# Optimization experiments

Measured on AMD Instinct MI355X. Metric: run time of the kernel, lower is better.

The kernel has to match this reference:

```python
import jax, jax.numpy as jnp
import numpy as np

D_MODEL = 1024
D_STATE = 16
D_CONV = 4
EXPAND = 2
D_INNER = EXPAND * D_MODEL          # 2048
DT_RANK = D_MODEL // 16             # 64 ('auto' in mamba_ssm)
B_SZ = 2
SEQ = 1024


def setup_inputs() -> dict:
    key = jax.random.key(0)
    ks = jax.random.split(key, 8)
    g = lambda k, shape, scale: (jax.random.normal(k, shape, dtype=jnp.float32) * scale)
    x = jax.random.normal(ks[0], (B_SZ, SEQ, D_MODEL), dtype=jnp.float32)
    in_proj_w = g(ks[1], (2 * D_INNER, D_MODEL), D_MODEL ** -0.5)
    conv_w = g(ks[2], (D_INNER, 1, D_CONV), D_CONV ** -0.5)
    conv_b = jnp.zeros((D_INNER,), jnp.float32)
    x_proj_w = g(ks[3], (DT_RANK + 2 * D_STATE, D_INNER), D_INNER ** -0.5)
    dt_proj_w = g(ks[4], (D_INNER, DT_RANK), DT_RANK ** -0.5)
    # dt bias initialized so softplus(bias) ~ [1e-3, 0.1] like mamba_ssm
    dt_proj_b = jax.random.uniform(ks[5], (D_INNER,), jnp.float32, -6.0, -2.0)
    # S4D-real init: A = -(1..d_state) per channel
    A_log = jnp.log(jnp.tile(jnp.arange(1, D_STATE + 1, dtype=jnp.float32), (D_INNER, 1)))
    D = jnp.ones((D_INNER,), jnp.float32)
    out_proj_w = g(ks[6], (D_MODEL, D_INNER), D_INNER ** -0.5)
    return dict(x=x, in_proj_w=in_proj_w, conv_w=conv_w, conv_b=conv_b,
                x_proj_w=x_proj_w, dt_proj_w=dt_proj_w, dt_proj_b=dt_proj_b,
                A_log=A_log, D=D, out_proj_w=out_proj_w)


def _mamba(x, in_proj_w, conv_w, conv_b, x_proj_w, dt_proj_w, dt_proj_b, A_log, D, out_proj_w):
    Bt, L, _ = x.shape
    # input projection -> [B, L, 2*d_inner], split into conv branch u and gate z
    xz = jnp.einsum('bld,ed->ble', x, in_proj_w)
    u, z = jnp.split(xz, 2, axis=-1)
    # causal depthwise conv1d over time
    uc = jnp.transpose(u, (0, 2, 1))  # [B, d_inner, L]
    uc = jax.lax.conv_general_dilated(
        uc, conv_w, window_strides=(1,), padding=[(D_CONV - 1, 0)],
        feature_group_count=D_INNER, dimension_numbers=('NCH', 'OIH', 'NCH'))
    u = jax.nn.silu(jnp.transpose(uc, (0, 2, 1)) + conv_b)  # [B, L, d_inner]
    # data-dependent SSM parameters
    x_dbl = jnp.einsum('bld,ed->ble', u, x_proj_w)  # [B, L, dt_rank + 2*d_state]
    dt, Bmat, Cmat = jnp.split(x_dbl, [DT_RANK, DT_RANK + D_STATE], axis=-1)
    delta = jax.nn.softplus(jnp.einsum('blr,dr->bld', dt, dt_proj_w) + dt_proj_b)
    A = -jnp.exp(A_log)  # [d_inner, d_state], strictly negative

    def step(h, inp):
        d_t, B_t, C_t, u_t = inp  # [B,d_inner],[B,d_state],[B,d_state],[B,d_inner]
        dA = jnp.exp(d_t[:, :, None] * A)                       # [B, d_inner, d_state]
        h = dA * h + (d_t * u_t)[:, :, None] * B_t[:, None, :]  # discretized update
        y = jnp.einsum('bdn,bn->bd', h, C_t)
        return h, y

    h0 = jnp.zeros((Bt, D_INNER, D_STATE), x.dtype)
    xs = (jnp.swapaxes(delta, 0, 1), jnp.swapaxes(Bmat, 0, 1),
          jnp.swapaxes(Cmat, 0, 1), jnp.swapaxes(u, 0, 1))
    _, ys = jax.lax.scan(step, h0, xs)
    y = jnp.swapaxes(ys, 0, 1) + u * D   # skip connection D*u
    y = y * jax.nn.silu(z)               # gated output
    return jnp.einsum('bld,ed->ble', y, out_proj_w)


def reference(x, in_proj_w, conv_w, conv_b, x_proj_w, dt_proj_w, dt_proj_b, A_log, D, out_proj_w):
    # ResidualMamba: x + Mamba(x)
    return x + _mamba(x, in_proj_w, conv_w, conv_b, x_proj_w, dt_proj_w, dt_proj_b, A_log, D, out_proj_w)
```

## Files before the change

kernel.cpp:

```cpp
#include <hip/hip_runtime.h>
#include <hip/hip_bf16.h>
#include <math.h>

#define D_MODEL 1024
#define D_STATE 16
#define D_CONV  4
#define D_INNER 2048
#define DT_RANK 64
#define B_SZ    2
#define SEQ     1024
#define ML      (B_SZ * SEQ)

typedef unsigned short ushort_t;
typedef __attribute__((ext_vector_type(8))) short s8v;
typedef __attribute__((ext_vector_type(4))) float f4v;

__device__ __forceinline__ float softplus_f(float v) {
    return (v > 20.f) ? v : log1pf(__expf(v));
}

__global__ __launch_bounds__(256) void split_bf16_tiled(
    const float* __restrict__ A, ushort_t* __restrict__ H, ushort_t* __restrict__ L,
    int Kd, int ktlog, int total)
{
    int t = blockIdx.x * 256 + threadIdx.x;
    if (t >= total) return;
    int kslot = t & 3;
    int r  = (t >> 2) & 127;
    int tl = t >> 9;
    int kt = tl & ((1 << ktlog) - 1);
    int rt = tl >> ktlog;
    int row = rt * 128 + r;
    int col = (kt << 5) + kslot * 8;

    const float* src = &A[(size_t)row * Kd + col];
    float4 v0 = *reinterpret_cast<const float4*>(src);
    float4 v1 = *reinterpret_cast<const float4*>(src + 4);
    float f[8] = {v0.x, v0.y, v0.z, v0.w, v1.x, v1.y, v1.z, v1.w};
    s8v hv, lv;
#pragma unroll
    for (int j = 0; j < 8; ++j) {
        unsigned int ub = __float_as_uint(f[j]);
        unsigned int hb = (ub + 0x7fffu + ((ub >> 16) & 1u)) >> 16;
        float hf = __uint_as_float(hb << 16);
        float g  = f[j] - hf;
        unsigned int ug = __float_as_uint(g);
        unsigned int lb = (ug + 0x7fffu + ((ug >> 16) & 1u)) >> 16;
        hv[j] = (short)hb;
        lv[j] = (short)lb;
    }
    *reinterpret_cast<s8v*>(&H[(size_t)t * 8]) = hv;
    *reinterpret_cast<s8v*>(&L[(size_t)t * 8]) = lv;
}

template <int WTM, bool RES>
__global__ __launch_bounds__(256) void gemm_mfma_split(
    const ushort_t* __restrict__ Ah, const ushort_t* __restrict__ Al,
    const ushort_t* __restrict__ Bh, const ushort_t* __restrict__ Bl,
    const float* __restrict__ Rres,
    float* __restrict__ C, int ldc, int K)
{
    constexpr int BM  = WTM * 32;
    constexpr int CPW = BM / 64;
    __shared__ short AhL[BM * 32], AlL[BM * 32];
    __shared__ short BhL[128 * 32], BlL[128 * 32];

    const int tid = threadIdx.x;
    const int l = tid & 63;
    const int w = tid >> 6;
    const int m0 = blockIdx.y * BM;
    const int n0 = blockIdx.x * 128;
    const int wm = (w >> 1) * (WTM * 16);
    const int wn = (w & 1) * 64;

    const int ktiles = K >> 5;
    size_t abase = (size_t)(m0 >> 7) * ktiles * 4096 + (size_t)(m0 & 127) * 32;
    size_t bbase = (size_t)(n0 >> 7) * ktiles * 4096;

    f4v acc[WTM][4] = {};

    for (int kt = 0; kt < ktiles; ++kt) {
#pragma unroll
        for (int i = 0; i < CPW; ++i) {
            int ci = w * CPW + i;
            __builtin_amdgcn_global_load_lds(
                (const __attribute__((address_space(1))) unsigned int*)(Ah + abase + ci * 512 + l * 8),
                (__attribute__((address_space(3))) unsigned int*)&AhL[ci * 512], 16, 0, 0);
            __builtin_amdgcn_global_load_lds(
                (const __attribute__((address_space(1))) unsigned int*)(Al + abase + ci * 512 + l * 8),
                (__attribute__((address_space(3))) unsigned int*)&AlL[ci * 512], 16, 0, 0);
        }
#pragma unroll
        for (int i = 0; i < 2; ++i) {
            int ci = w * 2 + i;
            __builtin_amdgcn_global_load_lds(
                (const __attribute__((address_space(1))) unsigned int*)(Bh + bbase + ci * 512 + l * 8),
                (__attribute__((address_space(3))) unsigned int*)&BhL[ci * 512], 16, 0, 0);
            __builtin_amdgcn_global_load_lds(
                (const __attribute__((address_space(1))) unsigned int*)(Bl + bbase + ci * 512 + l * 8),
                (__attribute__((address_space(3))) unsigned int*)&BlL[ci * 512], 16, 0, 0);
        }
        asm volatile("s_waitcnt vmcnt(0)" ::: "memory");
        __syncthreads();

        s8v fah[WTM], fal[WTM], fbh[4], fbl[4];
        const int fo = (l & 15) * 32 + (l >> 4) * 8;
#pragma unroll
        for (int tr = 0; tr < WTM; ++tr) {
            fah[tr] = *reinterpret_cast<const s8v*>(&AhL[(wm + tr * 16) * 32 + fo]);
            fal[tr] = *reinterpret_cast<const s8v*>(&AlL[(wm + tr * 16) * 32 + fo]);
        }
#pragma unroll
        for (int tc = 0; tc < 4; ++tc) {
            fbh[tc] = *reinterpret_cast<const s8v*>(&BhL[(wn + tc * 16) * 32 + fo]);
            fbl[tc] = *reinterpret_cast<const s8v*>(&BlL[(wn + tc * 16) * 32 + fo]);
        }

#pragma unroll
        for (int tr = 0; tr < WTM; ++tr)
#pragma unroll
            for (int tc = 0; tc < 4; ++tc) {
                f4v c = acc[tr][tc];
                c = __builtin_amdgcn_mfma_f32_16x16x32_bf16(fah[tr], fbh[tc], c, 0, 0, 0);
                c = __builtin_amdgcn_mfma_f32_16x16x32_bf16(fah[tr], fbl[tc], c, 0, 0, 0);
                c = __builtin_amdgcn_mfma_f32_16x16x32_bf16(fal[tr], fbh[tc], c, 0, 0, 0);
                acc[tr][tc] = c;
            }
        __syncthreads();
        abase += 4096;
        bbase += 4096;
    }

    const int mb = m0 + wm + ((l >> 4) << 2);
    const int nb = n0 + wn + (l & 15);
#pragma unroll
    for (int tr = 0; tr < WTM; ++tr)
#pragma unroll
        for (int tc = 0; tc < 4; ++tc)
#pragma unroll
            for (int r = 0; r < 4; ++r) {
                int m = mb + tr * 16 + r;
                int n = nb + tc * 16;
                float v = acc[tr][tc][r];
                if (RES) v += Rres[(size_t)m * ldc + n];
                C[(size_t)m * ldc + n] = v;
            }
}

template <int BM, int BN, int TM, int TN, int ACT, bool BIAS>
__global__ __launch_bounds__(256) void gemm_tn(
    const float* __restrict__ A, int lda,
    const float* __restrict__ W, int ldw,
    const float* __restrict__ bias,
    float* __restrict__ C, int ldc,
    int K)
{
    constexpr int BK = 16;
    constexpr int LDA_S = BM + 4;
    constexpr int LDB_S = BN + 4;
    constexpr int RSUB = TM / 4;
    constexpr int CSUB = TN / 4;
    constexpr int NTX = BN / TN;
    constexpr int AF4 = BM * 4 / 256;
    constexpr int BF4 = BN * 4 / 256;
    static_assert((BM / TM) * (BN / TN) == 256, "256 threads");

    __shared__ float As[BK][LDA_S];
    __shared__ float Bs[BK][LDB_S];

    const int tid = threadIdx.x;
    const int tx = tid % NTX;
    const int ty = tid / NTX;
    const int m0 = blockIdx.y * BM;
    const int n0 = blockIdx.x * BN;

    float acc[TM][TN] = {};
    float4 pa[AF4], pb[BF4];

#pragma unroll
    for (int i = 0; i < AF4; ++i) {
        int f = tid + i * 256, row = f >> 2, kq = f & 3;
        pa[i] = *reinterpret_cast<const float4*>(&A[(size_t)(m0 + row) * lda + kq * 4]);
    }
#pragma unroll
    for (int i = 0; i < BF4; ++i) {
        int f = tid + i * 256, row = f >> 2, kq = f & 3;
        pb[i] = *reinterpret_cast<const float4*>(&W[(size_t)(n0 + row) * ldw + kq * 4]);
    }

    for (int k0 = 0; k0 < K; k0 += BK) {
#pragma unroll
        for (int i = 0; i < AF4; ++i) {
            int f = tid + i * 256, row = f >> 2, kq = f & 3;
            As[kq * 4 + 0][row] = pa[i].x; As[kq * 4 + 1][row] = pa[i].y;
            As[kq * 4 + 2][row] = pa[i].z; As[kq * 4 + 3][row] = pa[i].w;
        }
#pragma unroll
        for (int i = 0; i < BF4; ++i) {
            int f = tid + i * 256, row = f >> 2, kq = f & 3;
            Bs[kq * 4 + 0][row] = pb[i].x; Bs[kq * 4 + 1][row] = pb[i].y;
            Bs[kq * 4 + 2][row] = pb[i].z; Bs[kq * 4 + 3][row] = pb[i].w;
        }
        __syncthreads();

        if (k0 + BK < K) {
#pragma unroll
            for (int i = 0; i < AF4; ++i) {
                int f = tid + i * 256, row = f >> 2, kq = f & 3;
                pa[i] = *reinterpret_cast<const float4*>(&A[(size_t)(m0 + row) * lda + k0 + BK + kq * 4]);
            }
#pragma unroll
            for (int i = 0; i < BF4; ++i) {
                int f = tid + i * 256, row = f >> 2, kq = f & 3;
                pb[i] = *reinterpret_cast<const float4*>(&W[(size_t)(n0 + row) * ldw + k0 + BK + kq * 4]);
            }
        }

#pragma unroll
        for (int kk = 0; kk < BK; ++kk) {
            float a[TM], b[TN];
#pragma unroll
            for (int r = 0; r < RSUB; ++r) {
                float4 av = *reinterpret_cast<const float4*>(&As[kk][r * (BM / RSUB) + ty * 4]);
                a[r * 4 + 0] = av.x; a[r * 4 + 1] = av.y; a[r * 4 + 2] = av.z; a[r * 4 + 3] = av.w;
            }
#pragma unroll
            for (int c = 0; c < CSUB; ++c) {
                float4 bv = *reinterpret_cast<const float4*>(&Bs[kk][c * (BN / CSUB) + tx * 4]);
                b[c * 4 + 0] = bv.x; b[c * 4 + 1] = bv.y; b[c * 4 + 2] = bv.z; b[c * 4 + 3] = bv.w;
            }
#pragma unroll
            for (int i = 0; i < TM; ++i)
#pragma unroll
                for (int j = 0; j < TN; ++j)
                    acc[i][j] = fmaf(a[i], b[j], acc[i][j]);
        }
        __syncthreads();
    }

#pragma unroll
    for (int i = 0; i < TM; ++i) {
        int r = i >> 2, ii = i & 3;
        int m = m0 + r * (BM / RSUB) + ty * 4 + ii;
#pragma unroll
        for (int c = 0; c < CSUB; ++c) {
            int n = n0 + c * (BN / CSUB) + tx * 4;
            float v0 = acc[i][c * 4 + 0], v1 = acc[i][c * 4 + 1];
            float v2 = acc[i][c * 4 + 2], v3 = acc[i][c * 4 + 3];
            if (BIAS) {
                float4 b4 = *reinterpret_cast<const float4*>(&bias[n]);
                v0 += b4.x; v1 += b4.y; v2 += b4.z; v3 += b4.w;
            }
            if (ACT == 1) {
                v0 = softplus_f(v0); v1 = softplus_f(v1);
                v2 = softplus_f(v2); v3 = softplus_f(v3);
            }
            *reinterpret_cast<float4*>(&C[(size_t)m * ldc + n]) = make_float4(v0, v1, v2, v3);
        }
    }
}

__global__ __launch_bounds__(256) void conv_silu(
    const float* __restrict__ xz,
    const float* __restrict__ cw,
    const float* __restrict__ cb,
    float* __restrict__ u)
{
    int idx = blockIdx.x * 256 + threadIdx.x;
    if (idx >= ML * (D_INNER / 4)) return;
    int d4  = idx & (D_INNER / 4 - 1);
    int row = idx >> 9;
    int l   = row & (SEQ - 1);

    const float* base = xz + (size_t)row * 4096 + d4 * 4;
    float xr[4][4];
    {
        float4 v = *reinterpret_cast<const float4*>(base);
        xr[0][0] = v.x; xr[0][1] = v.y; xr[0][2] = v.z; xr[0][3] = v.w;
    }
#pragma unroll
    for (int t = 1; t < 4; ++t) {
        float4 v = make_float4(0.f, 0.f, 0.f, 0.f);
        if (l >= t) v = *reinterpret_cast<const float4*>(base - (size_t)t * 4096);
        xr[t][0] = v.x; xr[t][1] = v.y; xr[t][2] = v.z; xr[t][3] = v.w;
    }
    float4 b4 = *reinterpret_cast<const float4*>(&cb[d4 * 4]);
    float bb[4] = {b4.x, b4.y, b4.z, b4.w};
    float out[4];
#pragma unroll
    for (int c = 0; c < 4; ++c) {
        float4 w = *reinterpret_cast<const float4*>(&cw[(d4 * 4 + c) * 4]);
        float s = bb[c];
        s = fmaf(w.w, xr[0][c], s);
        s = fmaf(w.z, xr[1][c], s);
        s = fmaf(w.y, xr[2][c], s);
        s = fmaf(w.x, xr[3][c], s);
        out[c] = s / (1.f + __expf(-s));
    }
    *reinterpret_cast<float4*>(&u[(size_t)row * 2048 + d4 * 4]) =
        make_float4(out[0], out[1], out[2], out[3]);
}

__global__ __launch_bounds__(256) void xproj_partial(
    const float* __restrict__ u,
    const float* __restrict__ W,
    float* __restrict__ part)
{
    __shared__ float Us[64][36];
    __shared__ float Ws[96][36];
    const int tid = threadIdx.x;
    const int tx = tid & 31;
    const int ty = tid >> 5;
    const int r0 = blockIdx.x * 64;
    const int kbase = blockIdx.y * 256;

    float acc[8][3] = {};

    for (int kc = kbase; kc < kbase + 256; kc += 32) {
#pragma unroll
        for (int i = 0; i < 2; ++i) {
            int f = tid + i * 256, row = f >> 3, kq = f & 7;
            *reinterpret_cast<float4*>(&Us[row][kq * 4]) =
                *reinterpret_cast<const float4*>(&u[(size_t)(r0 + row) * 2048 + kc + kq * 4]);
        }
#pragma unroll
        for (int i = 0; i < 3; ++i) {
            int f = tid + i * 256, row = f >> 3, kq = f & 7;
            *reinterpret_cast<float4*>(&Ws[row][kq * 4]) =
                *reinterpret_cast<const float4*>(&W[(size_t)row * 2048 + kc + kq * 4]);
        }
        __syncthreads();
#pragma unroll
        for (int k4 = 0; k4 < 32; k4 += 4) {
            float4 wv[3];
#pragma unroll
            for (int j = 0; j < 3; ++j)
                wv[j] = *reinterpret_cast<const float4*>(&Ws[tx + 32 * j][k4]);
#pragma unroll
            for (int i = 0; i < 8; ++i) {
                float4 uv = *reinterpret_cast<const float4*>(&Us[ty * 8 + i][k4]);
#pragma unroll
                for (int j = 0; j < 3; ++j) {
                    acc[i][j] = fmaf(uv.x, wv[j].x, acc[i][j]);
                    acc[i][j] = fmaf(uv.y, wv[j].y, acc[i][j]);
                    acc[i][j] = fmaf(uv.z, wv[j].z, acc[i][j]);
                    acc[i][j] = fmaf(uv.w, wv[j].w, acc[i][j]);
                }
            }
        }
        __syncthreads();
    }
#pragma unroll
    for (int i = 0; i < 8; ++i)
#pragma unroll
        for (int j = 0; j < 3; ++j)
            part[((size_t)blockIdx.y * ML + r0 + ty * 8 + i) * 96 + tx + 32 * j] = acc[i][j];
}

__global__ __launch_bounds__(256) void xproj_reduce(
    const float* __restrict__ part,
    float* __restrict__ xdbl)
{
    int i = blockIdx.x * 256 + threadIdx.x;
    if (i >= ML * 96 / 4) return;
    const float4* p4 = reinterpret_cast<const float4*>(part);
    float4 s = p4[i];
#pragma unroll
    for (int sgl = 1; sgl < 8; ++sgl) {
        float4 v = p4[(size_t)sgl * (ML * 96 / 4) + i];
        s.x += v.x; s.y += v.y; s.z += v.z; s.w += v.w;
    }
    reinterpret_cast<float4*>(xdbl)[i] = s;
}

#define CH 64

__device__ __forceinline__ float dpp_add(float x, const int ctrl_unused) { return x; }

__global__ __launch_bounds__(256) void scan_kernel(
    const float* __restrict__ delta,
    const float* __restrict__ u,
    const float* __restrict__ xdbl,
    const float* __restrict__ xz,
    const float* __restrict__ A_log,
    const float* __restrict__ Dvec,
    float* __restrict__ yg)
{
    __shared__ __align__(16) float sd[16][CH + 4], su[16][CH + 4],
                                   sB[16][CH + 4], sC[16][CH + 4];
    __shared__ __align__(16) float sy[CH][20];

    const int tid = threadIdx.x;
    const int b   = blockIdx.x >> 7;
    const int d0  = (blockIdx.x & 127) * 16;
    const int dch = tid >> 4;
    const int n   = tid & 15;

    const int sc4 = (tid & 3) * 4;
    const int slr = tid >> 2;

    const float Aval = -expf(A_log[(d0 + dch) * 16 + n]);
    const float Dsel = (n == 15) ? Dvec[d0 + dch] : 0.f;
    float h = 0.f;

    for (int l0 = 0; l0 < SEQ; l0 += CH) {
        {
            int row = b * SEQ + l0 + slr;
            float4 dv = *reinterpret_cast<const float4*>(&delta[(size_t)row * 2048 + d0 + sc4]);
            float4 uv = *reinterpret_cast<const float4*>(&u[(size_t)row * 2048 + d0 + sc4]);
            float4 Bv = *reinterpret_cast<const float4*>(&xdbl[(size_t)row * 96 + 64 + sc4]);
            float4 Cv = *reinterpret_cast<const float4*>(&xdbl[(size_t)row * 96 + 80 + sc4]);
            sd[sc4 + 0][slr] = dv.x; sd[sc4 + 1][slr] = dv.y; sd[sc4 + 2][slr] = dv.z; sd[sc4 + 3][slr] = dv.w;
            su[sc4 + 0][slr] = uv.x; su[sc4 + 1][slr] = uv.y; su[sc4 + 2][slr] = uv.z; su[sc4 + 3][slr] = uv.w;
            sB[sc4 + 0][slr] = Bv.x; sB[sc4 + 1][slr] = Bv.y; sB[sc4 + 2][slr] = Bv.z; sB[sc4 + 3][slr] = Bv.w;
            sC[sc4 + 0][slr] = Cv.x; sC[sc4 + 1][slr] = Cv.y; sC[sc4 + 2][slr] = Cv.z; sC[sc4 + 3][slr] = Cv.w;
        }
        __syncthreads();

        float pbuf[8];
#pragma unroll 2
        for (int l8 = 0; l8 < CH; l8 += 8) {
#pragma unroll
            for (int g = 0; g < 2; ++g) {
                const int l4 = l8 + g * 4;
                float4 d4 = *reinterpret_cast<const float4*>(&sd[dch][l4]);
                float4 u4 = *reinterpret_cast<const float4*>(&su[dch][l4]);
                float4 B4 = *reinterpret_cast<const float4*>(&sB[n][l4]);
                float4 C4 = *reinterpret_cast<const float4*>(&sC[n][l4]);
                float dts[4] = {d4.x, d4.y, d4.z, d4.w};
                float uus[4] = {u4.x, u4.y, u4.z, u4.w};
                float Bs4[4] = {B4.x, B4.y, B4.z, B4.w};
                float Cs4[4] = {C4.x, C4.y, C4.z, C4.w};
#pragma unroll
                for (int j = 0; j < 4; ++j) {
                    float dt = dts[j];
                    float dA = __expf(dt * Aval);
                    h = fmaf(dA, h, dt * uus[j] * Bs4[j]);
                    pbuf[g * 4 + j] = fmaf(uus[j], Dsel, h * Cs4[j]);
                }
            }
#pragma unroll
            for (int j = 0; j < 8; ++j) {
                float p = pbuf[j];
                p += __int_as_float(__builtin_amdgcn_update_dpp(0, __float_as_int(p), 0x111, 0xf, 0xf, true));
                p += __int_as_float(__builtin_amdgcn_update_dpp(0, __float_as_int(p), 0x112, 0xf, 0xf, true));
                p += __int_as_float(__builtin_amdgcn_update_dpp(0, __float_as_int(p), 0x114, 0xf, 0xf, true));
                p += __int_as_float(__builtin_amdgcn_update_dpp(0, __float_as_int(p), 0x118, 0xf, 0xf, true));
                pbuf[j] = p;
            }
            if (n == 15) {
#pragma unroll
                for (int j = 0; j < 8; ++j) sy[l8 + j][dch] = pbuf[j];
            }
        }
        __syncthreads();

        {
            int row = b * SEQ + l0 + slr;
            float4 ps = *reinterpret_cast<const float4*>(&sy[slr][sc4]);
            float4 zv = *reinterpret_cast<const float4*>(&xz[(size_t)row * 4096 + 2048 + d0 + sc4]);
            float o[4];
            float pp[4] = {ps.x, ps.y, ps.z, ps.w};
            float zzv[4] = {zv.x, zv.y, zv.z, zv.w};
#pragma unroll
            for (int q = 0; q < 4; ++q) {
                float zz = zzv[q];
                o[q] = pp[q] * (zz / (1.f + __expf(-zz)));
            }
            *reinterpret_cast<float4*>(&yg[(size_t)row * 2048 + d0 + sc4]) =
                make_float4(o[0], o[1], o[2], o[3]);
        }
        __syncthreads();
    }
}

extern "C" void kernel_launch(void* const* d_in, const int* in_sizes, int n_in,
                              void* d_out, int out_size, void* d_ws, size_t ws_size,
                              hipStream_t stream)
{
    const float* x         = (const float*)d_in[0];
    const float* in_proj_w = (const float*)d_in[1];
    const float* conv_w    = (const float*)d_in[2];
    const float* conv_b    = (const float*)d_in[3];
    const float* x_proj_w  = (const float*)d_in[4];
    const float* dt_proj_w = (const float*)d_in[5];
    const float* dt_proj_b = (const float*)d_in[6];
    const float* A_log     = (const float*)d_in[7];
    const float* Dvec      = (const float*)d_in[8];
    const float* out_proj_w= (const float*)d_in[9];
    float* out = (float*)d_out;

    float* ws    = (float*)d_ws;
    float* xz    = ws;
    float* u     = ws + 8388608;
    float* xdbl  = ws + 12582912;
    float* delta = ws + 12779520;
    float* part  = delta;
    float* yg    = ws + 16973824;

    ushort_t* bfb = (ushort_t*)(ws + 21168128);
    ushort_t* Xh  = bfb;
    ushort_t* Xl  = bfb + 2097152;
    ushort_t* Wih = bfb + 4194304;
    ushort_t* Wil = bfb + 8388608;
    ushort_t* Ygh = bfb;
    ushort_t* Ygl = bfb + 4194304;
    ushort_t* Woh = bfb + 8388608;
    ushort_t* Wol = bfb + 10485760;

    split_bf16_tiled<<<dim3(1024), 256, 0, stream>>>(x, Xh, Xl, 1024, 5, ML * 1024 / 8);
    split_bf16_tiled<<<dim3(2048), 256, 0, stream>>>(in_proj_w, Wih, Wil, 1024, 5, 4096 * 1024 / 8);

    gemm_mfma_split<4, false><<<dim3(32, 16), 256, 0, stream>>>(
        Xh, Xl, Wih, Wil, nullptr, xz, 4096, 1024);

    conv_silu<<<dim3(ML * (D_INNER / 4) / 256), 256, 0, stream>>>(xz, conv_w, conv_b, u);

    xproj_partial<<<dim3(32, 8), 256, 0, stream>>>(u, x_proj_w, part);
    xproj_reduce<<<dim3((ML * 96 / 4 + 255) / 256), 256, 0, stream>>>(part, xdbl);

    gemm_tn<128, 128, 8, 8, 1, true><<<dim3(16, 16), 256, 0, stream>>>(
        xdbl, 96, dt_proj_w, 64, dt_proj_b, delta, 2048, 64);

    scan_kernel<<<dim3(256), 256, 0, stream>>>(delta, u, xdbl, xz, A_log, Dvec, yg);

    split_bf16_tiled<<<dim3(2048), 256, 0, stream>>>(yg, Ygh, Ygl, 2048, 6, ML * 2048 / 8);
    split_bf16_tiled<<<dim3(1024), 256, 0, stream>>>(out_proj_w, Woh, Wol, 2048, 6, 1024 * 2048 / 8);

    gemm_mfma_split<2, true><<<dim3(8, 32), 256, 0, stream>>>(
        Ygh, Ygl, Woh, Wol, x, out, 1024, 2048);
}
```

Baseline: 385.2 us.

## Fuse dt_proj GEMM and softplus into the selective scan kernel

Drops the separate dt_proj GEMM and its 16 MB delta buffer. Each scan block now loads its 16 rows of dt_proj_w plus bias into shared memory, and for every 64-step chunk computes delta = softplus(dt·W + b) from the dt slice of xdbl. This removes a kernel launch and a full write and read of delta through global memory. The cost is extra FMA work and an extra barrier per chunk inside the latency-bound scan, which runs only 256 blocks.

```diff
diff --git a/kernel.cpp b/kernel.cpp
--- a/kernel.cpp
+++ b/kernel.cpp
@@ -147,119 +147,6 @@
             }
 }
 
-template <int BM, int BN, int TM, int TN, int ACT, bool BIAS>
-__global__ __launch_bounds__(256) void gemm_tn(
-    const float* __restrict__ A, int lda,
-    const float* __restrict__ W, int ldw,
-    const float* __restrict__ bias,
-    float* __restrict__ C, int ldc,
-    int K)
-{
-    constexpr int BK = 16;
-    constexpr int LDA_S = BM + 4;
-    constexpr int LDB_S = BN + 4;
-    constexpr int RSUB = TM / 4;
-    constexpr int CSUB = TN / 4;
-    constexpr int NTX = BN / TN;
-    constexpr int AF4 = BM * 4 / 256;
-    constexpr int BF4 = BN * 4 / 256;
-    static_assert((BM / TM) * (BN / TN) == 256, "256 threads");
-
-    __shared__ float As[BK][LDA_S];
-    __shared__ float Bs[BK][LDB_S];
-
-    const int tid = threadIdx.x;
-    const int tx = tid % NTX;
-    const int ty = tid / NTX;
-    const int m0 = blockIdx.y * BM;
-    const int n0 = blockIdx.x * BN;
-
-    float acc[TM][TN] = {};
-    float4 pa[AF4], pb[BF4];
-
-#pragma unroll
-    for (int i = 0; i < AF4; ++i) {
-        int f = tid + i * 256, row = f >> 2, kq = f & 3;
-        pa[i] = *reinterpret_cast<const float4*>(&A[(size_t)(m0 + row) * lda + kq * 4]);
-    }
-#pragma unroll
-    for (int i = 0; i < BF4; ++i) {
-        int f = tid + i * 256, row = f >> 2, kq = f & 3;
-        pb[i] = *reinterpret_cast<const float4*>(&W[(size_t)(n0 + row) * ldw + kq * 4]);
-    }
-
-    for (int k0 = 0; k0 < K; k0 += BK) {
-#pragma unroll
-        for (int i = 0; i < AF4; ++i) {
-            int f = tid + i * 256, row = f >> 2, kq = f & 3;
-            As[kq * 4 + 0][row] = pa[i].x; As[kq * 4 + 1][row] = pa[i].y;
-            As[kq * 4 + 2][row] = pa[i].z; As[kq * 4 + 3][row] = pa[i].w;
-        }
-#pragma unroll
-        for (int i = 0; i < BF4; ++i) {
-            int f = tid + i * 256, row = f >> 2, kq = f & 3;
-            Bs[kq * 4 + 0][row] = pb[i].x; Bs[kq * 4 + 1][row] = pb[i].y;
-            Bs[kq * 4 + 2][row] = pb[i].z; Bs[kq * 4 + 3][row] = pb[i].w;
-        }
-        __syncthreads();
-
-        if (k0 + BK < K) {
-#pragma unroll
-            for (int i = 0; i < AF4; ++i) {
-                int f = tid + i * 256, row = f >> 2, kq = f & 3;
-                pa[i] = *reinterpret_cast<const float4*>(&A[(size_t)(m0 + row) * lda + k0 + BK + kq * 4]);
-            }
-#pragma unroll
-            for (int i = 0; i < BF4; ++i) {
-                int f = tid + i * 256, row = f >> 2, kq = f & 3;
-                pb[i] = *reinterpret_cast<const float4*>(&W[(size_t)(n0 + row) * ldw + k0 + BK + kq * 4]);
-            }
-        }
-
-#pragma unroll
-        for (int kk = 0; kk < BK; ++kk) {
-            float a[TM], b[TN];
-#pragma unroll
-            for (int r = 0; r < RSUB; ++r) {
-                float4 av = *reinterpret_cast<const float4*>(&As[kk][r * (BM / RSUB) + ty * 4]);
-                a[r * 4 + 0] = av.x; a[r * 4 + 1] = av.y; a[r * 4 + 2] = av.z; a[r * 4 + 3] = av.w;
-            }
-#pragma unroll
-            for (int c = 0; c < CSUB; ++c) {
-                float4 bv = *reinterpret_cast<const float4*>(&Bs[kk][c * (BN / CSUB) + tx * 4]);
-                b[c * 4 + 0] = bv.x; b[c * 4 + 1] = bv.y; b[c * 4 + 2] = bv.z; b[c * 4 + 3] = bv.w;
-            }
-#pragma unroll
-            for (int i = 0; i < TM; ++i)
-#pragma unroll
-                for (int j = 0; j < TN; ++j)
-                    acc[i][j] = fmaf(a[i], b[j], acc[i][j]);
-        }
-        __syncthreads();
-    }
-
-#pragma unroll
-    for (int i = 0; i < TM; ++i) {
-        int r = i >> 2, ii = i & 3;
-        int m = m0 + r * (BM / RSUB) + ty * 4 + ii;
-#pragma unroll
-        for (int c = 0; c < CSUB; ++c) {
-            int n = n0 + c * (BN / CSUB) + tx * 4;
-            float v0 = acc[i][c * 4 + 0], v1 = acc[i][c * 4 + 1];
-            float v2 = acc[i][c * 4 + 2], v3 = acc[i][c * 4 + 3];
-            if (BIAS) {
-                float4 b4 = *reinterpret_cast<const float4*>(&bias[n]);
-                v0 += b4.x; v1 += b4.y; v2 += b4.z; v3 += b4.w;
-            }
-            if (ACT == 1) {
-                v0 = softplus_f(v0); v1 = softplus_f(v1);
-                v2 = softplus_f(v2); v3 = softplus_f(v3);
-            }
-            *reinterpret_cast<float4*>(&C[(size_t)m * ldc + n]) = make_float4(v0, v1, v2, v3);
-        }
-    }
-}
-
 __global__ __launch_bounds__(256) void conv_silu(
     const float* __restrict__ xz,
     const float* __restrict__ cw,
@@ -375,19 +262,21 @@
 
 #define CH 64
 
-__device__ __forceinline__ float dpp_add(float x, const int ctrl_unused) { return x; }
-
 __global__ __launch_bounds__(256) void scan_kernel(
-    const float* __restrict__ delta,
     const float* __restrict__ u,
     const float* __restrict__ xdbl,
     const float* __restrict__ xz,
     const float* __restrict__ A_log,
     const float* __restrict__ Dvec,
+    const float* __restrict__ dtw,
+    const float* __restrict__ dtb,
     float* __restrict__ yg)
 {
-    __shared__ __align__(16) float sd[16][CH + 4], su[16][CH + 4],
+    __shared__ __align__(16) float sdt[CH][68];
+    __shared__ __align__(16) float sdel[16][CH + 4], su16[16][CH + 4],
                                    sB[16][CH + 4], sC[16][CH + 4];
+    __shared__ __align__(16) float dtw_s[16][68];
+    __shared__ float db_s[16];
     __shared__ __align__(16) float sy[CH][20];
 
     const int tid = threadIdx.x;
@@ -399,21 +288,61 @@
     const int sc4 = (tid & 3) * 4;
     const int slr = tid >> 2;
 
+    {
+        int r = tid >> 4, c4 = (tid & 15) * 4;
+        *reinterpret_cast<float4*>(&dtw_s[r][c4]) =
+            *reinterpret_cast<const float4*>(&dtw[(size_t)(d0 + r) * 64 + c4]);
+        if (tid < 16) db_s[tid] = dtb[d0 + tid];
+    }
     const float Aval = -expf(A_log[(d0 + dch) * 16 + n]);
     const float Dsel = (n == 15) ? Dvec[d0 + dch] : 0.f;
     float h = 0.f;
+    __syncthreads();
 
     for (int l0 = 0; l0 < SEQ; l0 += CH) {
         {
+#pragma unroll
+            for (int i = 0; i < 4; ++i) {
+                int idx = tid + i * 256;
+                int rr = idx >> 4, c4 = (idx & 15) * 4;
+                *reinterpret_cast<float4*>(&sdt[rr][c4]) =
+                    *reinterpret_cast<const float4*>(&xdbl[(size_t)(b * SEQ + l0 + rr) * 96 + c4]);
+            }
             int row = b * SEQ + l0 + slr;
-            float4 dv = *reinterpret_cast<const float4*>(&delta[(size_t)row * 2048 + d0 + sc4]);
             float4 uv = *reinterpret_cast<const float4*>(&u[(size_t)row * 2048 + d0 + sc4]);
             float4 Bv = *reinterpret_cast<const float4*>(&xdbl[(size_t)row * 96 + 64 + sc4]);
             float4 Cv = *reinterpret_cast<const float4*>(&xdbl[(size_t)row * 96 + 80 + sc4]);
-            sd[sc4 + 0][slr] = dv.x; sd[sc4 + 1][slr] = dv.y; sd[sc4 + 2][slr] = dv.z; sd[sc4 + 3][slr] = dv.w;
-            su[sc4 + 0][slr] = uv.x; su[sc4 + 1][slr] = uv.y; su[sc4 + 2][slr] = uv.z; su[sc4 + 3][slr] = uv.w;
-            sB[sc4 + 0][slr] = Bv.x; sB[sc4 + 1][slr] = Bv.y; sB[sc4 + 2][slr] = Bv.z; sB[sc4 + 3][slr] = Bv.w;
-            sC[sc4 + 0][slr] = Cv.x; sC[sc4 + 1][slr] = Cv.y; sC[sc4 + 2][slr] = Cv.z; sC[sc4 + 3][slr] = Cv.w;
+            su16[sc4 + 0][slr] = uv.x; su16[sc4 + 1][slr] = uv.y;
+            su16[sc4 + 2][slr] = uv.z; su16[sc4 + 3][slr] = uv.w;
+            sB[sc4 + 0][slr] = Bv.x; sB[sc4 + 1][slr] = Bv.y;
+            sB[sc4 + 2][slr] = Bv.z; sB[sc4 + 3][slr] = Bv.w;
+            sC[sc4 + 0][slr] = Cv.x; sC[sc4 + 1][slr] = Cv.y;
+            sC[sc4 + 2][slr] = Cv.z; sC[sc4 + 3][slr] = Cv.w;
+        }
+        __syncthreads();
+
+        {
+            float4 s0 = make_float4(0.f, 0.f, 0.f, 0.f), s1 = s0, s2 = s0, s3 = s0;
+#pragma unroll
+            for (int k4 = 0; k4 < 64; k4 += 4) {
+                float4 dv = *reinterpret_cast<const float4*>(&sdt[slr][k4]);
+                float4 w0 = *reinterpret_cast<const float4*>(&dtw_s[sc4 + 0][k4]);
+                float4 w1 = *reinterpret_cast<const float4*>(&dtw_s[sc4 + 1][k4]);
+                float4 w2 = *reinterpret_cast<const float4*>(&dtw_s[sc4 + 2][k4]);
+                float4 w3 = *reinterpret_cast<const float4*>(&dtw_s[sc4 + 3][k4]);
+                s0.x = fmaf(dv.x, w0.x, s0.x); s0.y = fmaf(dv.y, w0.y, s0.y);
+                s0.z = fmaf(dv.z, w0.z, s0.z); s0.w = fmaf(dv.w, w0.w, s0.w);
+                s1.x = fmaf(dv.x, w1.x, s1.x); s1.y = fmaf(dv.y, w1.y, s1.y);
+                s1.z = fmaf(dv.z, w1.z, s1.z); s1.w = fmaf(dv.w, w1.w, s1.w);
+                s2.x = fmaf(dv.x, w2.x, s2.x); s2.y = fmaf(dv.y, w2.y, s2.y);
+                s2.z = fmaf(dv.z, w2.z, s2.z); s2.w = fmaf(dv.w, w2.w, s2.w);
+                s3.x = fmaf(dv.x, w3.x, s3.x); s3.y = fmaf(dv.y, w3.y, s3.y);
+                s3.z = fmaf(dv.z, w3.z, s3.z); s3.w = fmaf(dv.w, w3.w, s3.w);
+            }
+            sdel[sc4 + 0][slr] = softplus_f((s0.x + s0.y) + (s0.z + s0.w) + db_s[sc4 + 0]);
+            sdel[sc4 + 1][slr] = softplus_f((s1.x + s1.y) + (s1.z + s1.w) + db_s[sc4 + 1]);
+            sdel[sc4 + 2][slr] = softplus_f((s2.x + s2.y) + (s2.z + s2.w) + db_s[sc4 + 2]);
+            sdel[sc4 + 3][slr] = softplus_f((s3.x + s3.y) + (s3.z + s3.w) + db_s[sc4 + 3]);
         }
         __syncthreads();
 
@@ -423,8 +352,8 @@
 #pragma unroll
             for (int g = 0; g < 2; ++g) {
                 const int l4 = l8 + g * 4;
-                float4 d4 = *reinterpret_cast<const float4*>(&sd[dch][l4]);
-                float4 u4 = *reinterpret_cast<const float4*>(&su[dch][l4]);
+                float4 d4 = *reinterpret_cast<const float4*>(&sdel[dch][l4]);
+                float4 u4 = *reinterpret_cast<const float4*>(&su16[dch][l4]);
                 float4 B4 = *reinterpret_cast<const float4*>(&sB[n][l4]);
                 float4 C4 = *reinterpret_cast<const float4*>(&sC[n][l4]);
                 float dts[4] = {d4.x, d4.y, d4.z, d4.w};
@@ -494,8 +423,7 @@
     float* xz    = ws;
     float* u     = ws + 8388608;
     float* xdbl  = ws + 12582912;
-    float* delta = ws + 12779520;
-    float* part  = delta;
+    float* part  = ws + 12779520;
     float* yg    = ws + 16973824;
 
     ushort_t* bfb = (ushort_t*)(ws + 21168128);
@@ -519,10 +447,8 @@
     xproj_partial<<<dim3(32, 8), 256, 0, stream>>>(u, x_proj_w, part);
     xproj_reduce<<<dim3((ML * 96 / 4 + 255) / 256), 256, 0, stream>>>(part, xdbl);
 
-    gemm_tn<128, 128, 8, 8, 1, true><<<dim3(16, 16), 256, 0, stream>>>(
-        xdbl, 96, dt_proj_w, 64, dt_proj_b, delta, 2048, 64);
-
-    scan_kernel<<<dim3(256), 256, 0, stream>>>(delta, u, xdbl, xz, A_log, Dvec, yg);
+    scan_kernel<<<dim3(256), 256, 0, stream>>>(
+        u, xdbl, xz, A_log, Dvec, dt_proj_w, dt_proj_b, yg);
 
     split_bf16_tiled<<<dim3(2048), 256, 0, stream>>>(yg, Ygh, Ygl, 2048, 6, ML * 2048 / 8);
     split_bf16_tiled<<<dim3(1024), 256, 0, stream>>>(out_proj_w, Woh, Wol, 2048, 6, 1024 * 2048 / 8);
```

Result: faster. 351.2 us (-8.8%).
